# Kernel tuning notes

Hardware: AMD Instinct MI355X
Metric: run time of the kernel (lower is better)

Reference implementation:

```python
import jax, jax.numpy as jnp
import numpy as np

N_NODES = 100000
N_EDGES = 1600000
N_GRAPHS = 256
F_IN = 54


def setup_inputs() -> dict:
    key = jax.random.key(0)
    ks = jax.random.split(key, 16)
    x = jax.random.normal(ks[0], (N_NODES, F_IN), dtype=jnp.float32)
    edge_index = jax.random.randint(ks[1], (2, N_EDGES), 0, N_NODES, dtype=jnp.int32)
    batch = jnp.sort(jax.random.randint(ks[2], (N_NODES,), 0, N_GRAPHS, dtype=jnp.int32))

    def lin(k, fi, fo):
        kw, kb = jax.random.split(k)
        lim = 1.0 / np.sqrt(fi)
        W = jax.random.uniform(kw, (fi, fo), minval=-lim, maxval=lim, dtype=jnp.float32)
        b = jax.random.uniform(kb, (fo,), minval=-lim, maxval=lim, dtype=jnp.float32)
        return W, b

    W1, b1 = lin(ks[3], 54, 54)
    W2, b2 = lin(ks[4], 54, 108)
    W3, b3 = lin(ks[5], 108, 216)
    Wf1, bf1 = lin(ks[6], 216, 1024)
    Wf2, bf2 = lin(ks[7], 1024, 128)
    return {"x": x, "edge_index": edge_index, "batch": batch,
            "W1": W1, "b1": b1, "W2": W2, "b2": b2, "W3": W3, "b3": b3,
            "Wf1": Wf1, "bf1": bf1, "Wf2": Wf2, "bf2": bf2}


def _gcn_norm(edge_index, n):
    # add self-loops, symmetric degree normalization (PyG GCNConv default)
    loop = jnp.arange(n, dtype=edge_index.dtype)
    row = jnp.concatenate([edge_index[0], loop])
    col = jnp.concatenate([edge_index[1], loop])
    deg = jax.ops.segment_sum(jnp.ones_like(col, dtype=jnp.float32), col, num_segments=n)
    dinv = jnp.where(deg > 0, jax.lax.rsqrt(deg), 0.0)
    norm = dinv[row] * dinv[col]
    return row, col, norm


def _gcn_conv(x, row, col, norm, W, b, n):
    h = x @ W                                  # [N, Fout]
    msg = h[row] * norm[:, None]               # [E+N, Fout] gather + scale
    out = jax.ops.segment_sum(msg, col, num_segments=n)  # scatter-add
    return out + b


def reference(x, edge_index, batch, W1, b1, W2, b2, W3, b3, Wf1, bf1, Wf2, bf2):
    n = x.shape[0]
    row, col, norm = _gcn_norm(edge_index, n)
    h = jax.nn.relu(_gcn_conv(x, row, col, norm, W1, b1, n))
    h = jax.nn.relu(_gcn_conv(h, row, col, norm, W2, b2, n))
    h = jax.nn.relu(_gcn_conv(h, row, col, norm, W3, b3, n))
    # global mean pool per graph
    sums = jax.ops.segment_sum(h, batch, num_segments=N_GRAPHS)
    cnts = jax.ops.segment_sum(jnp.ones((n,), jnp.float32), batch, num_segments=N_GRAPHS)
    pooled = sums / jnp.maximum(cnts, 1.0)[:, None]   # [G, 216]
    g = jax.nn.relu(pooled @ Wf1 + bf1)               # dropout = identity (eval)
    return g @ Wf2 + bf2                              # [G, 128]
```

## Files before the change

### kernel.cpp

```cpp
#include <hip/hip_runtime.h>


typedef _Float16 f16;
typedef _Float16 f16x2 __attribute__((ext_vector_type(2)));
typedef _Float16 f16x8 __attribute__((ext_vector_type(8)));
typedef float f32x4 __attribute__((ext_vector_type(4)));

static __host__ __device__ inline int cdiv(int a, int b) { return (a + b - 1) / b; }

constexpr int BSPAN = 512;
constexpr int EPB   = 4096;
constexpr int EPT   = EPB / 256;

__device__ __forceinline__ void wpack_one(const float* W, f16* Wb, int K, int F,
                                          int KT, int idx) {
    int j = idx & 7;
    int lane = (idx >> 3) & 63;
    int fi = idx >> 9;
    int kt = fi % KT;
    int nt = fi / KT;
    int k = kt * 32 + (lane >> 4) * 8 + j;
    int nn = nt * 16 + (lane & 15);
    Wb[idx] = (k < K && nn < F) ? (f16)W[k * F + nn] : (f16)0.f;
}

__global__ __launch_bounds__(256) void k_init(
        const int* __restrict__ batch, int* __restrict__ start,
        float* __restrict__ psum, int* __restrict__ bktCnt, int* __restrict__ bktCur,
        const int* __restrict__ col,
        const float* __restrict__ W1, const float* __restrict__ W2,
        const float* __restrict__ W3, f16* __restrict__ w1b,
        f16* __restrict__ w2b, f16* __restrict__ w3b,
        int e, int nb, int n, int g) {
    __shared__ int hist[256];
    int t = threadIdx.x;
    int i = blockIdx.x * blockDim.x + t;
    hist[t] = 0;
    __syncthreads();
    int ebase = blockIdx.x * EPB;
#pragma unroll
    for (int j = 0; j < EPT; j++) {
        int idx = ebase + j * 256 + t;
        if (idx < e) atomicAdd(&hist[col[idx] >> 9], 1);
    }
    if (i < g * 216) psum[i] = 0.f;
    if (i < 256) bktCur[i] = 0;
    constexpr int T1 = 4 * 2 * 512;
    constexpr int T2 = 7 * 2 * 512;
    constexpr int T3 = 14 * 4 * 512;
    if (i < T1) wpack_one(W1, w1b, 54, 54, 2, i);
    else if (i < T1 + T2) wpack_one(W2, w2b, 54, 108, 2, i - T1);
    else if (i < T1 + T2 + T3) wpack_one(W3, w3b, 108, 216, 4, i - T1 - T2);
    if (i < n) {
        int b = batch[i];
        int bp = (i == 0) ? -1 : batch[i - 1];
        for (int gg = bp + 1; gg <= b; gg++) start[gg] = i;
        if (i == n - 1)
            for (int gg = b + 1; gg <= g; gg++) start[gg] = n;
    }
    __syncthreads();
    if (t < nb && hist[t] > 0) atomicAdd(&bktCnt[t], hist[t]);
}

__device__ __forceinline__ int scan256_ex(int* sbuf, int v, int t) {
    sbuf[t] = v;
    __syncthreads();
    for (int off = 1; off < 256; off <<= 1) {
        int x = sbuf[t];
        int y = (t >= off) ? sbuf[t - off] : 0;
        __syncthreads();
        sbuf[t] = x + y;
        __syncthreads();
    }
    return sbuf[t] - v;
}

__global__ __launch_bounds__(256) void k_bkt_part(const int* __restrict__ row,
                                                  const int* __restrict__ col,
                                                  const int* __restrict__ bktCnt,
                                                  int* bktCur, unsigned int* __restrict__ ebuf,
                                                  int e, int nb) {
    __shared__ int sbuf[256];
    __shared__ int hist[256];
    __shared__ int base[256];
    __shared__ int lcur[256];
    int t = threadIdx.x;
    int boff = scan256_ex(sbuf, (t < nb) ? bktCnt[t] : 0, t);
    hist[t] = 0; lcur[t] = 0;
    __syncthreads();
    int bs = blockIdx.x * EPB;
    unsigned int pk[EPT];
    int b[EPT];
#pragma unroll
    for (int j = 0; j < EPT; j++) {
        int idx = bs + j * 256 + t;
        if (idx < e) {
            int c = col[idx];
            pk[j] = ((unsigned int)(c & (BSPAN - 1)) << 17) | (unsigned int)row[idx];
            b[j] = c >> 9;
            atomicAdd(&hist[b[j]], 1);
        } else b[j] = -1;
    }
    __syncthreads();
    if (t < nb && hist[t] > 0) base[t] = boff + atomicAdd(&bktCur[t], hist[t]);
    __syncthreads();
#pragma unroll
    for (int j = 0; j < EPT; j++) {
        if (b[j] >= 0) {
            int lofs = atomicAdd(&lcur[b[j]], 1);
            ebuf[base[b[j]] + lofs] = pk[j];
        }
    }
}

__global__ __launch_bounds__(256) void k_bkt_build(const unsigned int* __restrict__ ebuf,
                                                   const int* __restrict__ bktCnt,
                                                   int* __restrict__ rowptr,
                                                   float* __restrict__ dinv,
                                                   int* __restrict__ eSrc,
                                                   const float* __restrict__ x,
                                                   f16* __restrict__ xs,
                                                   int n, int nb) {
    __shared__ int sbuf[256];
    __shared__ int hist[BSPAN];
    __shared__ int cur[BSPAN];
    __shared__ float sdinv[BSPAN];
    int t = threadIdx.x;
    int bkt = blockIdx.x;

    int boff_ex = scan256_ex(sbuf, (t < nb) ? bktCnt[t] : 0, t);
    __shared__ int boff_s, cnt_s;
    if (t == bkt) boff_s = boff_ex;
    if (t == 0) cnt_s = bktCnt[bkt];
    hist[t] = 0; hist[t + 256] = 0;
    __syncthreads();
    int es = boff_s, ee = boff_s + cnt_s;

    {
        int i = es + t;
        for (; i + 3 * 256 < ee; i += 4 * 256) {
            unsigned p0 = ebuf[i], p1 = ebuf[i + 256], p2 = ebuf[i + 512], p3 = ebuf[i + 768];
            atomicAdd(&hist[p0 >> 17], 1);
            atomicAdd(&hist[p1 >> 17], 1);
            atomicAdd(&hist[p2 >> 17], 1);
            atomicAdd(&hist[p3 >> 17], 1);
        }
        for (; i < ee; i += 256) atomicAdd(&hist[ebuf[i] >> 17], 1);
    }
    __syncthreads();

    int h0 = hist[2 * t], h1 = hist[2 * t + 1];
    __syncthreads();
    int ex = scan256_ex(sbuf, h0 + h1, t);
    int e0 = es + ex, e1 = e0 + h0;

    int node0 = bkt * BSPAN;
    int n0 = node0 + 2 * t, n1 = node0 + 2 * t + 1;
    float d0 = rsqrtf((float)(h0 + 1)), d1 = rsqrtf((float)(h1 + 1));
    if (n0 <= n) rowptr[n0] = e0;
    if (n1 <= n) rowptr[n1] = e1;
    if (n0 < n) dinv[n0] = d0;
    if (n1 < n) dinv[n1] = d1;
    sdinv[2 * t] = d0; sdinv[2 * t + 1] = d1;
    cur[2 * t] = e0; cur[2 * t + 1] = e1;
    __syncthreads();

    {
        int i = es + t;
        for (; i + 3 * 256 < ee; i += 4 * 256) {
            unsigned p0 = ebuf[i], p1 = ebuf[i + 256], p2 = ebuf[i + 512], p3 = ebuf[i + 768];
            int s0 = atomicAdd(&cur[p0 >> 17], 1);
            int s1 = atomicAdd(&cur[p1 >> 17], 1);
            int s2 = atomicAdd(&cur[p2 >> 17], 1);
            int s3 = atomicAdd(&cur[p3 >> 17], 1);
            eSrc[s0] = (int)(p0 & 0x1FFFFu);
            eSrc[s1] = (int)(p1 & 0x1FFFFu);
            eSrc[s2] = (int)(p2 & 0x1FFFFu);
            eSrc[s3] = (int)(p3 & 0x1FFFFu);
        }
        for (; i < ee; i += 256) {
            unsigned int p = ebuf[i];
            int slot = atomicAdd(&cur[p >> 17], 1);
            eSrc[slot] = (int)(p & 0x1FFFFu);
        }
    }

    for (int idx = t; idx < BSPAN * 27; idx += 256) {
        int nl = idx / 27;
        int c = idx - nl * 27;
        int node = node0 + nl;
        if (node < n) {
            float d = sdinv[nl];
            float2 v = *reinterpret_cast<const float2*>(x + (long long)node * 54 + c * 2);
            f16x2 h;
            h[0] = (f16)(v.x * d);
            h[1] = (f16)(v.y * d);
            *reinterpret_cast<f16x2*>(xs + (long long)node * 64 + c * 2) = h;
        }
    }
}

template <int F, int RS>
__global__ __launch_bounds__(256) void k_gatherw(
        const int* __restrict__ rowptr, const int* __restrict__ eSrc,
        const float* __restrict__ dinv, const f16* __restrict__ hs,
        f16* __restrict__ out, int n) {
    constexpr int CGN = RS / 8;
    constexpr int EPW = 64 / CGN;
    int wave = threadIdx.x >> 6;
    int lane = threadIdx.x & 63;
    int eslot = lane / CGN;
    int cg = lane & (CGN - 1);
    int node = blockIdx.x * 4 + wave;
    if (node >= n) return;
    int ch0 = cg * 8;
    int lim = F - ch0;
    if (lim > 8) lim = 8;
    if (lim < 0) lim = 0;

    int rs_ = rowptr[node], re = rowptr[node + 1];
    float di = dinv[node];
    int deg = re - rs_;
    int myidx = 0;
    if (lane < deg) myidx = eSrc[rs_ + lane];

    const f16x8* src = reinterpret_cast<const f16x8*>(hs);
    float acc[8];
#pragma unroll
    for (int j = 0; j < 8; j++) acc[j] = 0.f;

    if (eslot == 0) {
        f16x8 v = src[(long long)node * CGN + cg];
#pragma unroll
        for (int j = 0; j < 8; j++) acc[j] += (float)v[j];
    }

    int nfull = deg < 64 ? deg : 64;
    for (int base = 0; base < nfull; base += 8 * EPW) {
        int sidx[8];
#pragma unroll
        for (int u = 0; u < 8; u++) {
            int idx = base + u * EPW + eslot;
            sidx[u] = __shfl(myidx, idx < 63 ? idx : 63);
        }
        f16x8 v[8];
#pragma unroll
        for (int u = 0; u < 8; u++) {
            int idx = base + u * EPW + eslot;
            if (idx < nfull) v[u] = src[(long long)sidx[u] * CGN + cg];
        }
#pragma unroll
        for (int u = 0; u < 8; u++) {
            int idx = base + u * EPW + eslot;
            if (idx < nfull) {
#pragma unroll
                for (int j = 0; j < 8; j++) acc[j] += (float)v[u][j];
            }
        }
    }
    for (int e = rs_ + 64 + eslot; e < re; e += EPW) {
        int s = eSrc[e];
        f16x8 v = src[(long long)s * CGN + cg];
#pragma unroll
        for (int j = 0; j < 8; j++) acc[j] += (float)v[j];
    }

#pragma unroll
    for (int j = 0; j < 8; j++)
        if (j >= lim) acc[j] = 0.f;
#pragma unroll
    for (int m = CGN; m < 64; m <<= 1)
#pragma unroll
        for (int j = 0; j < 8; j++) acc[j] += __shfl_xor(acc[j], m);

    if (eslot == 0) {
        f16x8 o;
#pragma unroll
        for (int j = 0; j < 8; j++) o[j] = (f16)(acc[j] * di);
        *reinterpret_cast<f16x8*>(out + (long long)node * RS + ch0) = o;
    }
}

template <int F, int KTILES, int NTILES, int FOUT, int OSTR>
__global__ __launch_bounds__(256) void k_gcn_fused(
        const int* __restrict__ rowptr, const int* __restrict__ eSrc,
        const float* __restrict__ dinv, const f16* __restrict__ hs,
        const f16* __restrict__ Wb, const float* __restrict__ bias,
        f16* __restrict__ outh, int n) {
    constexpr int KPAD = KTILES * 32;
    constexpr int KP   = KPAD + 8;
    constexpr int CGN  = KPAD / 8;
    constexpr int EPH  = 32 / CGN;

    __shared__ __align__(16) f16 a_lds[64 * KP];

    int t = threadIdx.x;
    int node0 = blockIdx.x * 64;
    int w = t >> 6;
    int lane = t & 63;
    int half = lane >> 5;
    int l = lane & 31;
    int eslot = l / CGN;
    int cg = l & (CGN - 1);
    int ch0 = cg * 8;
    int lim = F - ch0;
    if (lim > 8) lim = 8;
    if (lim < 0) lim = 0;
    int lbase = half * 32;

    const f16x8* src = reinterpret_cast<const f16x8*>(hs);
    int nodeBase = node0 + w * 16;

    for (int i = 0; i < 8; i++) {
        int node = nodeBase + 2 * i + half;
        float acc[8];
#pragma unroll
        for (int j = 0; j < 8; j++) acc[j] = 0.f;
        float di = 0.f;

        if (node < n) {
            int rs_ = rowptr[node], re = rowptr[node + 1];
            di = dinv[node];
            int deg = re - rs_;
            int myidx = 0;
            if (l < deg) myidx = eSrc[rs_ + l];

            if (eslot == 0) {
                f16x8 v = src[(long long)node * CGN + cg];
#pragma unroll
                for (int j = 0; j < 8; j++) acc[j] += (float)v[j];
            }

            int nfull = deg < 32 ? deg : 32;
            if (nfull > 0) {
                int sidx[8];
#pragma unroll
                for (int u = 0; u < 8; u++) {
                    int idx = u * EPH + eslot;
                    sidx[u] = __shfl(myidx, lbase + (idx < 31 ? idx : 31));
                }
                f16x8 v[8];
#pragma unroll
                for (int u = 0; u < 8; u++) {
                    int idx = u * EPH + eslot;
                    if (idx < nfull) v[u] = src[(long long)sidx[u] * CGN + cg];
                }
#pragma unroll
                for (int u = 0; u < 8; u++) {
                    int idx = u * EPH + eslot;
                    if (idx < nfull) {
#pragma unroll
                        for (int j = 0; j < 8; j++) acc[j] += (float)v[u][j];
                    }
                }
            }
            for (int e = rs_ + 32 + eslot; e < re; e += EPH) {
                int s = eSrc[e];
                f16x8 v = src[(long long)s * CGN + cg];
#pragma unroll
                for (int j = 0; j < 8; j++) acc[j] += (float)v[j];
            }

#pragma unroll
            for (int j = 0; j < 8; j++)
                if (j >= lim) acc[j] = 0.f;
#pragma unroll
            for (int m = CGN; m < 32; m <<= 1)
#pragma unroll
                for (int j = 0; j < 8; j++) acc[j] += __shfl_xor(acc[j], m);
        }

        if (eslot == 0) {
            f16x8 o;
#pragma unroll
            for (int j = 0; j < 8; j++) o[j] = (f16)(acc[j] * di);
            *reinterpret_cast<f16x8*>(&a_lds[(w * 16 + 2 * i + half) * KP + ch0]) = o;
        }
    }
    __syncthreads();

    int quad = lane >> 4;
    int col = lane & 15;

    f16x8 afr[KTILES];
#pragma unroll
    for (int kt = 0; kt < KTILES; kt++)
        afr[kt] = *reinterpret_cast<const f16x8*>(
            &a_lds[(16 * w + col) * KP + kt * 32 + quad * 8]);

    int nodeC = node0 + 16 * w + quad * 4;
    float dv[4];
#pragma unroll
    for (int r = 0; r < 4; r++) {
        int nd = nodeC + r;
        dv[r] = (nd < n) ? dinv[nd] : 0.f;
    }

    const f16x8* wb = reinterpret_cast<const f16x8*>(Wb);
#pragma unroll
    for (int nt = 0; nt < NTILES; nt++) {
        f16x8 bfr[KTILES];
#pragma unroll
        for (int kt = 0; kt < KTILES; kt++)
            bfr[kt] = wb[(nt * KTILES + kt) * 64 + lane];
        f32x4 acc = {0.f, 0.f, 0.f, 0.f};
#pragma unroll
        for (int kt = 0; kt < KTILES; kt++)
            acc = __builtin_amdgcn_mfma_f32_16x16x32_f16(afr[kt], bfr[kt], acc, 0, 0, 0);

        int ch = nt * 16 + col;
        if (ch < FOUT) {
            float bval = bias[ch];
#pragma unroll
            for (int r = 0; r < 4; r++) {
                int nd = nodeC + r;
                if (nd < n)
                    outh[(long long)nd * OSTR + ch] =
                        (f16)(fmaxf(acc[r] + bval, 0.f) * dv[r]);
            }
        }
    }
}

template <int KTILES, int NTILES, int K, int FOUT>
__global__ __launch_bounds__(256) void k_gemm_pool(
        const f16* __restrict__ in, const f16* __restrict__ Wb,
        const float* __restrict__ bias, const int* __restrict__ batch,
        float* __restrict__ psum, int n) {
    constexpr int KPAD = KTILES * 32;
    constexpr int KP   = KPAD + 8;
    constexpr int V8   = KPAD / 8;
    constexpr int NSLOT = 4;

    __shared__ f16 a_lds[64 * KP];
    __shared__ float psum_l[NSLOT * FOUT];

    int t = threadIdx.x;
    int node0 = blockIdx.x * 64;

    const f16x8* inp = reinterpret_cast<const f16x8*>(in);
    for (int f = t; f < 64 * V8; f += 256) {
        int node = f / V8;
        int v = f - node * V8;
        f16x8 val = {};
        if (node0 + node < n) val = inp[(long long)(node0 + node) * V8 + v];
        *reinterpret_cast<f16x8*>(&a_lds[node * KP + v * 8]) = val;
    }
    for (int i = t; i < NSLOT * FOUT; i += 256) psum_l[i] = 0.f;
    __syncthreads();

    int w = t >> 6;
    int lane = t & 63;
    int quad = lane >> 4;
    int col = lane & 15;

    f16x8 afr[KTILES];
#pragma unroll
    for (int kt = 0; kt < KTILES; kt++)
        afr[kt] = *reinterpret_cast<const f16x8*>(
            &a_lds[(16 * w + col) * KP + kt * 32 + quad * 8]);

    int nodeC = node0 + 16 * w + quad * 4;
    int gb[4];
#pragma unroll
    for (int r = 0; r < 4; r++) {
        int nd = nodeC + r;
        gb[r] = (nd < n) ? batch[nd] : -1;
    }
    int g0 = batch[node0];

    const f16x8* wb = reinterpret_cast<const f16x8*>(Wb);
#pragma unroll
    for (int nt = 0; nt < NTILES; nt++) {
        f16x8 bfr[KTILES];
#pragma unroll
        for (int kt = 0; kt < KTILES; kt++)
            bfr[kt] = wb[(nt * KTILES + kt) * 64 + lane];
        f32x4 acc = {0.f, 0.f, 0.f, 0.f};
#pragma unroll
        for (int kt = 0; kt < KTILES; kt++)
            acc = __builtin_amdgcn_mfma_f32_16x16x32_f16(afr[kt], bfr[kt], acc, 0, 0, 0);

        int ch = nt * 16 + col;
        if (ch < FOUT) {
            float bval = bias[ch];
            if (gb[0] == gb[3] && gb[0] >= 0) {
                float s = fmaxf(acc[0] + bval, 0.f) + fmaxf(acc[1] + bval, 0.f)
                        + fmaxf(acc[2] + bval, 0.f) + fmaxf(acc[3] + bval, 0.f);
                int slot = gb[0] - g0;
                if (slot < NSLOT) atomicAdd(&psum_l[slot * FOUT + ch], s);
                else atomicAdd(&psum[gb[0] * FOUT + ch], s);
            } else {
#pragma unroll
                for (int r = 0; r < 4; r++) {
                    if (gb[r] < 0) continue;
                    float v = fmaxf(acc[r] + bval, 0.f);
                    int slot = gb[r] - g0;
                    if (slot < NSLOT) atomicAdd(&psum_l[slot * FOUT + ch], v);
                    else atomicAdd(&psum[gb[r] * FOUT + ch], v);
                }
            }
        }
    }

    __syncthreads();
    int lastNode = node0 + 63;
    if (lastNode >= n) lastNode = n - 1;
    int nsl = batch[lastNode] - g0 + 1;
    if (nsl > NSLOT) nsl = NSLOT;
    for (int f = t; f < nsl * FOUT; f += 256) {
        float v = psum_l[f];
        if (v != 0.f) atomicAdd(&psum[(g0 + f / FOUT) * FOUT + (f % FOUT)], v);
    }
}

__global__ void k_fc1(const float* __restrict__ P, const int* __restrict__ start,
                      const float* __restrict__ W, const float* __restrict__ bias,
                      float* __restrict__ out) {
    int row = blockIdx.x >> 2;
    int o = (blockIdx.x & 3) * 256 + threadIdx.x;
    int cnt = start[row + 1] - start[row];
    float scale = 1.0f / fmaxf((float)cnt, 1.0f);
    __shared__ float prow[216];
    if (threadIdx.x < 216) prow[threadIdx.x] = P[row * 216 + threadIdx.x] * scale;
    __syncthreads();
    float acc = bias[o];
    for (int k = 0; k < 216; k++) acc += prow[k] * W[k * 1024 + o];
    out[row * 1024 + o] = fmaxf(acc, 0.f);
}
__global__ void k_fc2(const float* __restrict__ G, const float* __restrict__ W,
                      const float* __restrict__ bias, float* __restrict__ out) {
    int row = blockIdx.x;
    int o = threadIdx.x;
    __shared__ float grow[1024];
    for (int k = threadIdx.x; k < 1024; k += 128) grow[k] = G[row * 1024 + k];
    __syncthreads();
    float acc = bias[o];
    for (int k = 0; k < 1024; k++) acc += grow[k] * W[k * 128 + o];
    out[row * 128 + o] = acc;
}

extern "C" void kernel_launch(void* const* d_in, const int* in_sizes, int n_in,
                              void* d_out, int out_size, void* d_ws, size_t ws_size,
                              hipStream_t stream) {
    const float* x     = (const float*)d_in[0];
    const int*   ei    = (const int*)d_in[1];
    const int*   batch = (const int*)d_in[2];
    const float* W1  = (const float*)d_in[3];
    const float* b1  = (const float*)d_in[4];
    const float* W2  = (const float*)d_in[5];
    const float* b2  = (const float*)d_in[6];
    const float* W3  = (const float*)d_in[7];
    const float* b3  = (const float*)d_in[8];
    const float* Wf1 = (const float*)d_in[9];
    const float* bf1 = (const float*)d_in[10];
    const float* Wf2 = (const float*)d_in[11];
    const float* bf2 = (const float*)d_in[12];
    float* out = (float*)d_out;

    const int N = in_sizes[0] / 54;
    const int E = in_sizes[1] / 2;
    const int G = 256;
    const int* row = ei;
    const int* col = ei + E;
    const int NB = cdiv(N, BSPAN);
    const int NBLK_A = cdiv(E, EPB);

    char* ws = (char*)d_ws;
    size_t off = 0;
    auto carve = [&](size_t bytes) {
        void* p = ws + off;
        off += (bytes + 255) & ~(size_t)255;
        return p;
    };
    int*   rowptr  = (int*)carve((size_t)(N + 1) * 4);
    int*   bktCnt  = (int*)carve(256 * 4);
    int*   bktCur  = (int*)carve(256 * 4);
    int*   eSrc    = (int*)carve((size_t)E * 4);
    float* dinv    = (float*)carve((size_t)N * 4);
    f16*   xs      = (f16*)carve((size_t)N * 64 * 2);
    f16*   hsbuf   = (f16*)carve((size_t)N * 128 * 2);
    f16*   bufA    = (f16*)carve((size_t)N * 128 * 2);
    unsigned int* ebuf = (unsigned int*)carve((size_t)E * 4);
    float* psum    = (float*)carve((size_t)G * 216 * 4);
    float* gbuf    = (float*)carve((size_t)G * 1024 * 4);
    int*   start   = (int*)carve((size_t)(G + 1) * 4);
    f16*   w1b     = (f16*)carve((size_t)4 * 2 * 512 * 2);
    f16*   w2b     = (f16*)carve((size_t)7 * 2 * 512 * 2);
    f16*   w3b     = (f16*)carve((size_t)14 * 4 * 512 * 2);

    const int T = 256;
    hipMemsetAsync(bktCnt, 0, 256 * 4, stream);

    int gInit = cdiv(N, T) > NBLK_A ? cdiv(N, T) : NBLK_A;
    k_init<<<gInit, T, 0, stream>>>(batch, start, psum, bktCnt, bktCur, col,
                                    W1, W2, W3, w1b, w2b, w3b, E, NB, N, G);

    k_bkt_part<<<NBLK_A, 256, 0, stream>>>(row, col, bktCnt, bktCur, ebuf, E, NB);
    k_bkt_build<<<NB, 256, 0, stream>>>(ebuf, bktCnt, rowptr, dinv, eSrc, x, xs, N, NB);

    const int GB = cdiv(N, 64);

    k_gcn_fused<54, 2, 4, 54, 64><<<GB, 256, 0, stream>>>(
        rowptr, eSrc, dinv, xs, w1b, b1, hsbuf, N);

    k_gcn_fused<54, 2, 7, 108, 128><<<GB, 256, 0, stream>>>(
        rowptr, eSrc, dinv, hsbuf, w2b, b2, bufA, N);

    k_gatherw<108, 128><<<cdiv(N, 4), 256, 0, stream>>>(rowptr, eSrc, dinv, bufA, hsbuf, N);
    k_gemm_pool<4, 14, 108, 216><<<GB, 256, 0, stream>>>(
        hsbuf, w3b, b3, batch, psum, N);

    k_fc1<<<G * 4, T, 0, stream>>>(psum, start, Wf1, bf1, gbuf);
    k_fc2<<<G, 128, 0, stream>>>(gbuf, Wf2, bf2, out);
}
```

Measured before the change: 399.2 us.

## Split x prescale into own kernel; double waves per block in fused GCN layers

```diff
diff --git a/kernel.cpp b/kernel.cpp
--- a/kernel.cpp
+++ b/kernel.cpp
@@ -118,13 +118,10 @@
                                                    int* __restrict__ rowptr,
                                                    float* __restrict__ dinv,
                                                    int* __restrict__ eSrc,
-                                                   const float* __restrict__ x,
-                                                   f16* __restrict__ xs,
                                                    int n, int nb) {
     __shared__ int sbuf[256];
     __shared__ int hist[BSPAN];
     __shared__ int cur[BSPAN];
-    __shared__ float sdinv[BSPAN];
     int t = threadIdx.x;
     int bkt = blockIdx.x;
 
@@ -156,12 +153,10 @@
 
     int node0 = bkt * BSPAN;
     int n0 = node0 + 2 * t, n1 = node0 + 2 * t + 1;
-    float d0 = rsqrtf((float)(h0 + 1)), d1 = rsqrtf((float)(h1 + 1));
     if (n0 <= n) rowptr[n0] = e0;
     if (n1 <= n) rowptr[n1] = e1;
-    if (n0 < n) dinv[n0] = d0;
-    if (n1 < n) dinv[n1] = d1;
-    sdinv[2 * t] = d0; sdinv[2 * t + 1] = d1;
+    if (n0 < n) dinv[n0] = rsqrtf((float)(h0 + 1));
+    if (n1 < n) dinv[n1] = rsqrtf((float)(h1 + 1));
     cur[2 * t] = e0; cur[2 * t + 1] = e1;
     __syncthreads();
 
@@ -184,20 +179,22 @@
             eSrc[slot] = (int)(p & 0x1FFFFu);
         }
     }
-
-    for (int idx = t; idx < BSPAN * 27; idx += 256) {
-        int nl = idx / 27;
-        int c = idx - nl * 27;
-        int node = node0 + nl;
-        if (node < n) {
-            float d = sdinv[nl];
-            float2 v = *reinterpret_cast<const float2*>(x + (long long)node * 54 + c * 2);
-            f16x2 h;
-            h[0] = (f16)(v.x * d);
-            h[1] = (f16)(v.y * d);
-            *reinterpret_cast<f16x2*>(xs + (long long)node * 64 + c * 2) = h;
-        }
-    }
+}
+
+template <int F, int RS>
+__global__ void k_prescale(const float* __restrict__ x, const float* __restrict__ dinv,
+                           f16* __restrict__ xs, int n) {
+    constexpr int CH = F / 2;
+    int idx = blockIdx.x * blockDim.x + threadIdx.x;
+    if (idx >= n * CH) return;
+    int node = idx / CH;
+    int c = idx - node * CH;
+    float d = dinv[node];
+    float2 v = *reinterpret_cast<const float2*>(x + (long long)node * F + c * 2);
+    f16x2 h;
+    h[0] = (f16)(v.x * d);
+    h[1] = (f16)(v.y * d);
+    *reinterpret_cast<f16x2*>(xs + (long long)node * RS + c * 2) = h;
 }
 
 template <int F, int RS>
@@ -282,7 +279,7 @@
 }
 
 template <int F, int KTILES, int NTILES, int FOUT, int OSTR>
-__global__ __launch_bounds__(256) void k_gcn_fused(
+__global__ __launch_bounds__(512) void k_gcn_fused(
         const int* __restrict__ rowptr, const int* __restrict__ eSrc,
         const float* __restrict__ dinv, const f16* __restrict__ hs,
         const f16* __restrict__ Wb, const float* __restrict__ bias,
@@ -291,6 +288,7 @@
     constexpr int KP   = KPAD + 8;
     constexpr int CGN  = KPAD / 8;
     constexpr int EPH  = 32 / CGN;
+    constexpr int NT0  = (NTILES + 1) / 2;
 
     __shared__ __align__(16) f16 a_lds[64 * KP];
 
@@ -309,9 +307,9 @@
     int lbase = half * 32;
 
     const f16x8* src = reinterpret_cast<const f16x8*>(hs);
-    int nodeBase = node0 + w * 16;
-
-    for (int i = 0; i < 8; i++) {
+    int nodeBase = node0 + w * 8;
+
+    for (int i = 0; i < 4; i++) {
         int node = nodeBase + 2 * i + half;
         float acc[8];
 #pragma unroll
@@ -374,11 +372,13 @@
             f16x8 o;
 #pragma unroll
             for (int j = 0; j < 8; j++) o[j] = (f16)(acc[j] * di);
-            *reinterpret_cast<f16x8*>(&a_lds[(w * 16 + 2 * i + half) * KP + ch0]) = o;
-        }
-    }
-    __syncthreads();
-
+            *reinterpret_cast<f16x8*>(&a_lds[(w * 8 + 2 * i + half) * KP + ch0]) = o;
+        }
+    }
+    __syncthreads();
+
+    int rw = w & 3;
+    int ng = w >> 2;
     int quad = lane >> 4;
     int col = lane & 15;
 
@@ -386,9 +386,9 @@
 #pragma unroll
     for (int kt = 0; kt < KTILES; kt++)
         afr[kt] = *reinterpret_cast<const f16x8*>(
-            &a_lds[(16 * w + col) * KP + kt * 32 + quad * 8]);
-
-    int nodeC = node0 + 16 * w + quad * 4;
+            &a_lds[(16 * rw + col) * KP + kt * 32 + quad * 8]);
+
+    int nodeC = node0 + 16 * rw + quad * 4;
     float dv[4];
 #pragma unroll
     for (int r = 0; r < 4; r++) {
@@ -399,6 +399,7 @@
     const f16x8* wb = reinterpret_cast<const f16x8*>(Wb);
 #pragma unroll
     for (int nt = 0; nt < NTILES; nt++) {
+        if ((nt < NT0) != (ng == 0)) continue;
         f16x8 bfr[KTILES];
 #pragma unroll
         for (int kt = 0; kt < KTILES; kt++)
@@ -597,14 +598,16 @@
                                     W1, W2, W3, w1b, w2b, w3b, E, NB, N, G);
 
     k_bkt_part<<<NBLK_A, 256, 0, stream>>>(row, col, bktCnt, bktCur, ebuf, E, NB);
-    k_bkt_build<<<NB, 256, 0, stream>>>(ebuf, bktCnt, rowptr, dinv, eSrc, x, xs, N, NB);
+    k_bkt_build<<<NB, 256, 0, stream>>>(ebuf, bktCnt, rowptr, dinv, eSrc, N, NB);
+
+    k_prescale<54, 64><<<cdiv(N * 27, T), T, 0, stream>>>(x, dinv, xs, N);
 
     const int GB = cdiv(N, 64);
 
-    k_gcn_fused<54, 2, 4, 54, 64><<<GB, 256, 0, stream>>>(
+    k_gcn_fused<54, 2, 4, 54, 64><<<GB, 512, 0, stream>>>(
         rowptr, eSrc, dinv, xs, w1b, b1, hsbuf, N);
 
-    k_gcn_fused<54, 2, 7, 108, 128><<<GB, 256, 0, stream>>>(
+    k_gcn_fused<54, 2, 7, 108, 128><<<GB, 512, 0, stream>>>(
         rowptr, eSrc, dinv, hsbuf, w2b, b2, bufA, N);
 
     k_gatherw<108, 128><<<cdiv(N, 4), 256, 0, stream>>>(rowptr, eSrc, dinv, bufA, hsbuf, N);
```

Result: faster. 383.3 us (-4.0%).
